# Kernel optimization log

Hardware: AMD Instinct MI355X
Metric: run time of the kernel (lower is better)

Reference implementation:

```python
import jax, jax.numpy as jnp
import numpy as np

D_MODEL = 1024
N_HEADS = 16
HEAD = D_MODEL // N_HEADS
SEQ_THRESH = 64
EPS = 1e-12  # F.normalize eps


def setup_inputs() -> dict:
    key = jax.random.key(0)
    ks = jax.random.split(key, 12)
    B, S = 2, 2048
    scale_init = float(np.log2(SEQ_THRESH ** 2 - SEQ_THRESH))
    return {
        "query": jax.random.normal(ks[0], (B, S, D_MODEL), dtype=jnp.float32),
        "key": jax.random.normal(ks[1], (B, S, D_MODEL), dtype=jnp.float32),
        "value": jax.random.normal(ks[2], (B, S, D_MODEL), dtype=jnp.float32),
        "mask": jax.random.randint(ks[3], (B, S), 0, 2, dtype=jnp.int32),
        "Wq": jax.random.normal(ks[4], (D_MODEL, D_MODEL), dtype=jnp.float32) * (1.0 / np.sqrt(D_MODEL)),
        "bq": jnp.zeros((D_MODEL,), dtype=jnp.float32),
        "Wk": jax.random.normal(ks[5], (D_MODEL, D_MODEL), dtype=jnp.float32) * (1.0 / np.sqrt(D_MODEL)),
        "bk": jnp.zeros((D_MODEL,), dtype=jnp.float32),
        "Wv": jax.random.normal(ks[6], (D_MODEL, D_MODEL), dtype=jnp.float32) * (1.0 / np.sqrt(D_MODEL)),
        "bv": jnp.zeros((D_MODEL,), dtype=jnp.float32),
        "Wo": jax.random.normal(ks[7], (D_MODEL, D_MODEL), dtype=jnp.float32) * (1.0 / np.sqrt(D_MODEL)),
        "bo": jnp.zeros((D_MODEL,), dtype=jnp.float32),
        "scale": jnp.asarray(scale_init, dtype=jnp.float32),
    }


def _split_heads(x):
    B, S, _ = x.shape
    return x.reshape(B, S, N_HEADS, HEAD).transpose(0, 2, 1, 3)  # [B,H,S,hd]


def _center_normalize(x):
    x = x - jnp.mean(x, axis=-1, keepdims=True)
    norm = jnp.linalg.norm(x, axis=-1, keepdims=True)
    return x / jnp.maximum(norm, EPS)


def reference(query, key, value, mask, Wq, bq, Wk, bk, Wv, bv, Wo, bo, scale):
    B, Sq, _ = query.shape
    Q = _split_heads(query @ Wq.T + bq)
    K = _split_heads(key @ Wk.T + bk)
    V = _split_heads(value @ Wv.T + bv)
    Q = _center_normalize(Q)
    K = _center_normalize(K)
    scores = scale * jnp.einsum("bhqd,bhkd->bhqk", Q, K)
    scores = jnp.where(mask[:, None, None, :] == 0, jnp.float32(-1e9), scores)
    attn = jax.nn.softmax(scores, axis=-1)  # [B,H,Sq,Sk]
    ctx = jnp.einsum("bhqk,bhkd->bhqd", attn, V)
    ctx = ctx.transpose(0, 2, 1, 3).reshape(B, Sq, D_MODEL)
    ctx = ctx @ Wo.T + bo
    return (ctx, attn)
```

## Files before the change

kernel.cpp:

```cpp
#include <hip/hip_runtime.h>
#include <math.h>

#define DM   1024
#define NH   16
#define HD   64
#define BATCH 2
#define SEQ  2048
#define MR   (BATCH*SEQ)

typedef __attribute__((ext_vector_type(8))) short bf16x8;
typedef __attribute__((ext_vector_type(4))) float f32x4;

__device__ __forceinline__ unsigned short f2bf(float x) {
    unsigned u = __builtin_bit_cast(unsigned, x);
    u = (u + 0x7FFFu + ((u >> 16) & 1u)) >> 16;
    return (unsigned short)u;
}
__device__ __forceinline__ float bf2f(unsigned short s) {
    unsigned u = ((unsigned)s) << 16;
    return __builtin_bit_cast(float, u);
}

__global__ __launch_bounds__(256) void convert_split(
    const float* __restrict__ src, unsigned short* __restrict__ hi,
    unsigned short* __restrict__ lo, int n4)
{
    int i = blockIdx.x * 256 + threadIdx.x;
    if (i >= n4) return;
    float4 v = ((const float4*)src)[i];
    float f[4] = {v.x, v.y, v.z, v.w};
    unsigned short h[4], l[4];
#pragma unroll
    for (int k = 0; k < 4; ++k) {
        h[k] = f2bf(f[k]);
        l[k] = f2bf(f[k] - bf2f(h[k]));
    }
    ((ushort4*)hi)[i] = make_ushort4(h[0], h[1], h[2], h[3]);
    ((ushort4*)lo)[i] = make_ushort4(l[0], l[1], l[2], l[3]);
}

__global__ __launch_bounds__(256) void convert_single(
    const float* __restrict__ src, unsigned short* __restrict__ dst, int n4)
{
    int i = blockIdx.x * 256 + threadIdx.x;
    if (i >= n4) return;
    float4 v = ((const float4*)src)[i];
    ((ushort4*)dst)[i] = make_ushort4(f2bf(v.x), f2bf(v.y), f2bf(v.z), f2bf(v.w));
}

template<int MODE>
__global__ __launch_bounds__(256) void proj_gemm(
    const unsigned short* __restrict__ Ahi, const unsigned short* __restrict__ Alo,
    const unsigned short* __restrict__ Bhi, const unsigned short* __restrict__ Blo,
    const float* __restrict__ bias,
    void* __restrict__ out0, unsigned short* __restrict__ out1)
{
    __shared__ __align__(16) short As[2][64][40];
    __shared__ __align__(16) short Bs[2][128][40];

    const int tid  = threadIdx.x;
    const int wave = tid >> 6, lane = tid & 63;
    const int quad = lane >> 4, lr = lane & 15;
    const int wy = wave >> 1, wx = wave & 1;
    const int m0 = blockIdx.x * 64, n0 = blockIdx.y * 128;

    f32x4 acc[2][4];
#pragma unroll
    for (int i = 0; i < 2; ++i)
#pragma unroll
        for (int j = 0; j < 4; ++j) acc[i][j] = (f32x4){0.f, 0.f, 0.f, 0.f};

    const int arow = tid >> 2, aseg = (tid & 3) * 8;
    const int brow = tid >> 1, bseg = (tid & 1) * 16;

    for (int k0 = 0; k0 < DM; k0 += 32) {
        __syncthreads();
        {
            const size_t ao = (size_t)(m0 + arow) * DM + k0 + aseg;
            *(uint4*)&As[0][arow][aseg] = *(const uint4*)&Ahi[ao];
            if (MODE == 0)
                *(uint4*)&As[1][arow][aseg] = *(const uint4*)&Alo[ao];
        }
        {
            const size_t bo = (size_t)(n0 + brow) * DM + k0 + bseg;
            *(uint4*)&Bs[0][brow][bseg]     = *(const uint4*)&Bhi[bo];
            *(uint4*)&Bs[0][brow][bseg + 8] = *(const uint4*)&Bhi[bo + 8];
            if (MODE == 0) {
                *(uint4*)&Bs[1][brow][bseg]     = *(const uint4*)&Blo[bo];
                *(uint4*)&Bs[1][brow][bseg + 8] = *(const uint4*)&Blo[bo + 8];
            }
        }
        __syncthreads();
        bf16x8 ah[2], al[2], bh[4], bl[4];
#pragma unroll
        for (int i = 0; i < 2; ++i) {
            ah[i] = *(const bf16x8*)&As[0][wy * 32 + i * 16 + lr][quad * 8];
            if (MODE == 0) al[i] = *(const bf16x8*)&As[1][wy * 32 + i * 16 + lr][quad * 8];
        }
#pragma unroll
        for (int j = 0; j < 4; ++j) {
            bh[j] = *(const bf16x8*)&Bs[0][wx * 64 + j * 16 + lr][quad * 8];
            if (MODE == 0) bl[j] = *(const bf16x8*)&Bs[1][wx * 64 + j * 16 + lr][quad * 8];
        }
#pragma unroll
        for (int i = 0; i < 2; ++i)
#pragma unroll
            for (int j = 0; j < 4; ++j) {
                acc[i][j] = __builtin_amdgcn_mfma_f32_16x16x32_bf16(ah[i], bh[j], acc[i][j], 0, 0, 0);
                if (MODE == 0) {
                    acc[i][j] = __builtin_amdgcn_mfma_f32_16x16x32_bf16(ah[i], bl[j], acc[i][j], 0, 0, 0);
                    acc[i][j] = __builtin_amdgcn_mfma_f32_16x16x32_bf16(al[i], bh[j], acc[i][j], 0, 0, 0);
                }
            }
    }

    float bj[4];
#pragma unroll
    for (int j = 0; j < 4; ++j) bj[j] = bias[n0 + wx * 64 + j * 16 + lr];

    if (MODE == 0) {
        unsigned short* Ohi = (unsigned short*)out0;
#pragma unroll
        for (int i = 0; i < 2; ++i) {
#pragma unroll
            for (int r = 0; r < 4; ++r) {
                float x[4];
#pragma unroll
                for (int j = 0; j < 4; ++j) x[j] = acc[i][j][r] + bj[j];
                float t = x[0] + x[1] + x[2] + x[3];
                t += __shfl_xor(t, 1, 16);
                t += __shfl_xor(t, 2, 16);
                t += __shfl_xor(t, 4, 16);
                t += __shfl_xor(t, 8, 16);
                const float mean = t * (1.0f / 64.0f);
                float ss = 0.f;
#pragma unroll
                for (int j = 0; j < 4; ++j) { x[j] -= mean; ss += x[j] * x[j]; }
                ss += __shfl_xor(ss, 1, 16);
                ss += __shfl_xor(ss, 2, 16);
                ss += __shfl_xor(ss, 4, 16);
                ss += __shfl_xor(ss, 8, 16);
                const float inv = 1.0f / fmaxf(sqrtf(ss), 1e-12f);
                const int row = m0 + wy * 32 + i * 16 + quad * 4 + r;
#pragma unroll
                for (int j = 0; j < 4; ++j) {
                    const float y = x[j] * inv;
                    const unsigned short hh = f2bf(y);
                    const unsigned short ll = f2bf(y - bf2f(hh));
                    const size_t o = (size_t)row * DM + n0 + wx * 64 + j * 16 + lr;
                    Ohi[o]  = hh;
                    out1[o] = ll;
                }
            }
        }
    } else if (MODE == 1) {
        unsigned short* Vg = (unsigned short*)out0;
        const int h = (n0 + wx * 64) >> 6;
#pragma unroll
        for (int i = 0; i < 2; ++i) {
            const int grow = m0 + wy * 32 + i * 16 + quad * 4;
            const int bb = grow >> 11, ss = grow & (SEQ - 1);
#pragma unroll
            for (int j = 0; j < 4; ++j) {
                const int d = j * 16 + lr;
                ushort4 pk;
                pk.x = f2bf(acc[i][j][0] + bj[j]);
                pk.y = f2bf(acc[i][j][1] + bj[j]);
                pk.z = f2bf(acc[i][j][2] + bj[j]);
                pk.w = f2bf(acc[i][j][3] + bj[j]);
                *(ushort4*)&Vg[((size_t)(bb * NH + h) * HD + d) * SEQ + ss] = pk;
            }
        }
    } else {
        float* O = (float*)out0;
#pragma unroll
        for (int i = 0; i < 2; ++i)
#pragma unroll
            for (int j = 0; j < 4; ++j)
#pragma unroll
                for (int r = 0; r < 4; ++r)
                    O[(size_t)(m0 + wy * 32 + i * 16 + quad * 4 + r) * DM +
                      n0 + wx * 64 + j * 16 + lr] = acc[i][j][r] + bj[j];
    }
}

__global__ __launch_bounds__(256) void attn_fused(
    const unsigned short* __restrict__ Qhi, const unsigned short* __restrict__ Qlo,
    const unsigned short* __restrict__ Khi, const unsigned short* __restrict__ Klo,
    const unsigned short* __restrict__ Vg,  const int* __restrict__ mask,
    const float* __restrict__ scale_p,
    float* __restrict__ attn, unsigned short* __restrict__ ctxb)
{
    __shared__ __align__(16) short KHs[64][72];
    __shared__ __align__(16) short KLs[64][72];
    __shared__ __align__(16) short Vs[64][72];
    __shared__ __align__(16) short Ps[64][72];
    __shared__ float mkf[64];

    const int tid = threadIdx.x;
    const int w = tid >> 6, lane = tid & 63;
    const int quad = lane >> 4, lr = lane & 15;

    const int lin = blockIdx.x;
    const int swz = (lin & 7) * 128 + (lin >> 3);
    const int b  = swz >> 9;
    const int h  = (swz >> 5) & 15;
    const int q0 = (swz & 31) * 64;

    const float scl = scale_p[0];
    const float s2 = scl * 1.44269504089f;
    const float c2 = -12.0f * 1.44269504089f;

    const int r0 = tid >> 3,        c0 = (tid & 7) * 8;
    const int r1 = (tid >> 3) + 32, c1 = (tid & 7) * 8;

    {
        const size_t base = ((size_t)(b * SEQ + q0)) * DM + h * HD;
        *(uint4*)&KHs[r0][c0] = *(const uint4*)&Qhi[base + (size_t)r0 * DM + c0];
        *(uint4*)&KHs[r1][c1] = *(const uint4*)&Qhi[base + (size_t)r1 * DM + c1];
        *(uint4*)&KLs[r0][c0] = *(const uint4*)&Qlo[base + (size_t)r0 * DM + c0];
        *(uint4*)&KLs[r1][c1] = *(const uint4*)&Qlo[base + (size_t)r1 * DM + c1];
    }
    __syncthreads();
    bf16x8 qh[2], ql[2];
#pragma unroll
    for (int kc = 0; kc < 2; ++kc) {
        qh[kc] = *(const bf16x8*)&KHs[w * 16 + lr][kc * 32 + quad * 8];
        ql[kc] = *(const bf16x8*)&KLs[w * 16 + lr][kc * 32 + quad * 8];
    }

    float rs[4] = {0.f, 0.f, 0.f, 0.f};

    for (int kt = 0; kt < SEQ / 64; ++kt) {
        const int kk = kt * 64;
        const size_t kb = ((size_t)(b * SEQ + kk)) * DM + h * HD;
        __syncthreads();
        *(uint4*)&KHs[r0][c0] = *(const uint4*)&Khi[kb + (size_t)r0 * DM + c0];
        *(uint4*)&KHs[r1][c1] = *(const uint4*)&Khi[kb + (size_t)r1 * DM + c1];
        *(uint4*)&KLs[r0][c0] = *(const uint4*)&Klo[kb + (size_t)r0 * DM + c0];
        *(uint4*)&KLs[r1][c1] = *(const uint4*)&Klo[kb + (size_t)r1 * DM + c1];
        if (tid < 64) mkf[tid] = mask[b * SEQ + kk + tid] ? c2 : -3.0e38f;
        __syncthreads();
#pragma unroll
        for (int j = 0; j < 4; ++j) {
            bf16x8 bh0 = *(const bf16x8*)&KHs[j * 16 + lr][quad * 8];
            bf16x8 bh1 = *(const bf16x8*)&KHs[j * 16 + lr][32 + quad * 8];
            bf16x8 bl0 = *(const bf16x8*)&KLs[j * 16 + lr][quad * 8];
            bf16x8 bl1 = *(const bf16x8*)&KLs[j * 16 + lr][32 + quad * 8];
            f32x4 sa = (f32x4){0.f, 0.f, 0.f, 0.f};
            sa = __builtin_amdgcn_mfma_f32_16x16x32_bf16(qh[0], bh0, sa, 0, 0, 0);
            sa = __builtin_amdgcn_mfma_f32_16x16x32_bf16(ql[0], bh0, sa, 0, 0, 0);
            sa = __builtin_amdgcn_mfma_f32_16x16x32_bf16(qh[0], bl0, sa, 0, 0, 0);
            sa = __builtin_amdgcn_mfma_f32_16x16x32_bf16(qh[1], bh1, sa, 0, 0, 0);
            sa = __builtin_amdgcn_mfma_f32_16x16x32_bf16(ql[1], bh1, sa, 0, 0, 0);
            sa = __builtin_amdgcn_mfma_f32_16x16x32_bf16(qh[1], bl1, sa, 0, 0, 0);
            const float mo = mkf[j * 16 + lr];
#pragma unroll
            for (int r = 0; r < 4; ++r)
                rs[r] += exp2f(fmaf(sa[r], s2, mo));
        }
    }

    float rinv[4];
#pragma unroll
    for (int r = 0; r < 4; ++r) {
        float t = rs[r];
        t += __shfl_xor(t, 1, 16);
        t += __shfl_xor(t, 2, 16);
        t += __shfl_xor(t, 4, 16);
        t += __shfl_xor(t, 8, 16);
        rinv[r] = 1.0f / fmaxf(t, 1e-30f);
    }

    f32x4 acc_o[4];
#pragma unroll
    for (int dt = 0; dt < 4; ++dt) acc_o[dt] = (f32x4){0.f, 0.f, 0.f, 0.f};

    for (int kt = 0; kt < SEQ / 64; ++kt) {
        const int kk = kt * 64;
        const size_t kb = ((size_t)(b * SEQ + kk)) * DM + h * HD;
        const size_t vb = ((size_t)((b * NH + h) * HD)) * SEQ + kk;
        __syncthreads();
        *(uint4*)&KHs[r0][c0] = *(const uint4*)&Khi[kb + (size_t)r0 * DM + c0];
        *(uint4*)&KHs[r1][c1] = *(const uint4*)&Khi[kb + (size_t)r1 * DM + c1];
        *(uint4*)&KLs[r0][c0] = *(const uint4*)&Klo[kb + (size_t)r0 * DM + c0];
        *(uint4*)&KLs[r1][c1] = *(const uint4*)&Klo[kb + (size_t)r1 * DM + c1];
        *(uint4*)&Vs[r0][c0]  = *(const uint4*)&Vg[vb + (size_t)r0 * SEQ + c0];
        *(uint4*)&Vs[r1][c1]  = *(const uint4*)&Vg[vb + (size_t)r1 * SEQ + c1];
        if (tid < 64) mkf[tid] = mask[b * SEQ + kk + tid] ? c2 : -3.0e38f;
        __syncthreads();
#pragma unroll
        for (int j = 0; j < 4; ++j) {
            bf16x8 bh0 = *(const bf16x8*)&KHs[j * 16 + lr][quad * 8];
            bf16x8 bh1 = *(const bf16x8*)&KHs[j * 16 + lr][32 + quad * 8];
            bf16x8 bl0 = *(const bf16x8*)&KLs[j * 16 + lr][quad * 8];
            bf16x8 bl1 = *(const bf16x8*)&KLs[j * 16 + lr][32 + quad * 8];
            f32x4 sa = (f32x4){0.f, 0.f, 0.f, 0.f};
            sa = __builtin_amdgcn_mfma_f32_16x16x32_bf16(qh[0], bh0, sa, 0, 0, 0);
            sa = __builtin_amdgcn_mfma_f32_16x16x32_bf16(ql[0], bh0, sa, 0, 0, 0);
            sa = __builtin_amdgcn_mfma_f32_16x16x32_bf16(qh[0], bl0, sa, 0, 0, 0);
            sa = __builtin_amdgcn_mfma_f32_16x16x32_bf16(qh[1], bh1, sa, 0, 0, 0);
            sa = __builtin_amdgcn_mfma_f32_16x16x32_bf16(ql[1], bh1, sa, 0, 0, 0);
            sa = __builtin_amdgcn_mfma_f32_16x16x32_bf16(qh[1], bl1, sa, 0, 0, 0);
            const float mo = mkf[j * 16 + lr];
#pragma unroll
            for (int r = 0; r < 4; ++r) {
                const float pn = exp2f(fmaf(sa[r], s2, mo)) * rinv[r];
                const int qrow = q0 + w * 16 + quad * 4 + r;
                attn[((size_t)(b * NH + h) * SEQ + qrow) * SEQ + kk + j * 16 + lr] = pn;
                Ps[w * 16 + quad * 4 + r][j * 16 + lr] = (short)f2bf(pn);
            }
        }
        bf16x8 pa0 = *(const bf16x8*)&Ps[w * 16 + lr][quad * 8];
        bf16x8 pa1 = *(const bf16x8*)&Ps[w * 16 + lr][32 + quad * 8];
#pragma unroll
        for (int dt = 0; dt < 4; ++dt) {
            bf16x8 bv0 = *(const bf16x8*)&Vs[dt * 16 + lr][quad * 8];
            bf16x8 bv1 = *(const bf16x8*)&Vs[dt * 16 + lr][32 + quad * 8];
            acc_o[dt] = __builtin_amdgcn_mfma_f32_16x16x32_bf16(pa0, bv0, acc_o[dt], 0, 0, 0);
            acc_o[dt] = __builtin_amdgcn_mfma_f32_16x16x32_bf16(pa1, bv1, acc_o[dt], 0, 0, 0);
        }
    }

#pragma unroll
    for (int dt = 0; dt < 4; ++dt)
#pragma unroll
        for (int r = 0; r < 4; ++r)
            ctxb[((size_t)(b * SEQ + q0 + w * 16 + quad * 4 + r)) * DM +
                 h * HD + dt * 16 + lr] = (unsigned short)f2bf(acc_o[dt][r]);
}

extern "C" void kernel_launch(void* const* d_in, const int* in_sizes, int n_in,
                              void* d_out, int out_size, void* d_ws, size_t ws_size,
                              hipStream_t stream)
{
    const float* query = (const float*)d_in[0];
    const float* key   = (const float*)d_in[1];
    const float* value = (const float*)d_in[2];
    const int*   mask  = (const int*)d_in[3];
    const float* Wq = (const float*)d_in[4];
    const float* bq = (const float*)d_in[5];
    const float* Wk = (const float*)d_in[6];
    const float* bk = (const float*)d_in[7];
    const float* Wv = (const float*)d_in[8];
    const float* bv = (const float*)d_in[9];
    const float* Wo = (const float*)d_in[10];
    const float* bo = (const float*)d_in[11];
    const float* scale = (const float*)d_in[12];

    float* out_ctx  = (float*)d_out;
    float* out_attn = out_ctx + (size_t)MR * DM;

    const size_t WSZ = (size_t)DM * DM;
    const size_t TSZ = (size_t)MR * DM;
    unsigned short* p = (unsigned short*)d_ws;
    unsigned short* Wq_hi = p; p += WSZ;
    unsigned short* Wq_lo = p; p += WSZ;
    unsigned short* Wk_hi = p; p += WSZ;
    unsigned short* Wk_lo = p; p += WSZ;
    unsigned short* Wv_b  = p; p += WSZ;
    unsigned short* Wo_b  = p; p += WSZ;
    unsigned short* Qn_hi = p; p += TSZ;
    unsigned short* Qn_lo = p; p += TSZ;
    unsigned short* Kn_hi = p; p += TSZ;
    unsigned short* Kn_lo = p; p += TSZ;
    unsigned short* Vg    = p; p += TSZ;
    unsigned short* ctxb  = Wq_hi;
    unsigned short* Ahi = (unsigned short*)out_attn;
    unsigned short* Alo = Ahi + TSZ;

    convert_split <<<1024, 256, 0, stream>>>(Wq, Wq_hi, Wq_lo, 262144);
    convert_split <<<1024, 256, 0, stream>>>(Wk, Wk_hi, Wk_lo, 262144);
    convert_single<<<1024, 256, 0, stream>>>(Wv, Wv_b, 262144);
    convert_single<<<1024, 256, 0, stream>>>(Wo, Wo_b, 262144);

    dim3 gg(MR / 64, DM / 128);

    convert_split <<<4096, 256, 0, stream>>>(query, Ahi, Alo, (int)(TSZ / 4));
    proj_gemm<0><<<gg, 256, 0, stream>>>(Ahi, Alo, Wq_hi, Wq_lo, bq, Qn_hi, Qn_lo);
    convert_split <<<4096, 256, 0, stream>>>(key, Ahi, Alo, (int)(TSZ / 4));
    proj_gemm<0><<<gg, 256, 0, stream>>>(Ahi, Alo, Wk_hi, Wk_lo, bk, Kn_hi, Kn_lo);
    convert_single<<<4096, 256, 0, stream>>>(value, Ahi, (int)(TSZ / 4));
    proj_gemm<1><<<gg, 256, 0, stream>>>(Ahi, nullptr, Wv_b, nullptr, bv, Vg, nullptr);

    attn_fused<<<dim3(SEQ / 64 * NH * BATCH), 256, 0, stream>>>(
        Qn_hi, Qn_lo, Kn_hi, Kn_lo, Vg, mask, scale, out_attn, ctxb);

    proj_gemm<2><<<gg, 256, 0, stream>>>(ctxb, nullptr, Wo_b, nullptr, bo, out_ctx, nullptr);
}
```

Measured before the change: 920.2 us.

## Fuse two-pass attention into one pass with deferred normalization and register prefetch

```diff
diff --git a/kernel.cpp b/kernel.cpp
--- a/kernel.cpp
+++ b/kernel.cpp
@@ -189,12 +189,13 @@
     const unsigned short* __restrict__ Khi, const unsigned short* __restrict__ Klo,
     const unsigned short* __restrict__ Vg,  const int* __restrict__ mask,
     const float* __restrict__ scale_p,
-    float* __restrict__ attn, unsigned short* __restrict__ ctxb)
+    float* __restrict__ attn, unsigned short* __restrict__ ctxb,
+    float* __restrict__ rowinv_g)
 {
     __shared__ __align__(16) short KHs[64][72];
     __shared__ __align__(16) short KLs[64][72];
     __shared__ __align__(16) short Vs[64][72];
-    __shared__ __align__(16) short Ps[64][72];
+    __shared__ __align__(16) short Ps[64][68];
     __shared__ float mkf[64];
 
     const int tid = threadIdx.x;
@@ -230,17 +231,48 @@
     }
 
     float rs[4] = {0.f, 0.f, 0.f, 0.f};
-
-    for (int kt = 0; kt < SEQ / 64; ++kt) {
+    f32x4 acc_o[4];
+#pragma unroll
+    for (int dt = 0; dt < 4; ++dt) acc_o[dt] = (f32x4){0.f, 0.f, 0.f, 0.f};
+
+    uint4 pKH0, pKH1, pKL0, pKL1, pV0, pV1;
+    int pmk = 0;
+
+    auto load_tile = [&](int kt) {
         const int kk = kt * 64;
         const size_t kb = ((size_t)(b * SEQ + kk)) * DM + h * HD;
-        __syncthreads();
-        *(uint4*)&KHs[r0][c0] = *(const uint4*)&Khi[kb + (size_t)r0 * DM + c0];
-        *(uint4*)&KHs[r1][c1] = *(const uint4*)&Khi[kb + (size_t)r1 * DM + c1];
-        *(uint4*)&KLs[r0][c0] = *(const uint4*)&Klo[kb + (size_t)r0 * DM + c0];
-        *(uint4*)&KLs[r1][c1] = *(const uint4*)&Klo[kb + (size_t)r1 * DM + c1];
-        if (tid < 64) mkf[tid] = mask[b * SEQ + kk + tid] ? c2 : -3.0e38f;
-        __syncthreads();
+        const size_t vb = ((size_t)((b * NH + h) * HD)) * SEQ + kk;
+        pKH0 = *(const uint4*)&Khi[kb + (size_t)r0 * DM + c0];
+        pKH1 = *(const uint4*)&Khi[kb + (size_t)r1 * DM + c1];
+        pKL0 = *(const uint4*)&Klo[kb + (size_t)r0 * DM + c0];
+        pKL1 = *(const uint4*)&Klo[kb + (size_t)r1 * DM + c1];
+        pV0  = *(const uint4*)&Vg[vb + (size_t)r0 * SEQ + c0];
+        pV1  = *(const uint4*)&Vg[vb + (size_t)r1 * SEQ + c1];
+        if (tid < 64) pmk = mask[b * SEQ + kk + tid];
+    };
+
+    load_tile(0);
+
+    for (int kt = 0; kt < SEQ / 64; ++kt) {
+        asm volatile("s_waitcnt lgkmcnt(0)" ::: "memory");
+        __builtin_amdgcn_s_barrier();
+        __builtin_amdgcn_sched_barrier(0);
+
+        *(uint4*)&KHs[r0][c0] = pKH0;
+        *(uint4*)&KHs[r1][c1] = pKH1;
+        *(uint4*)&KLs[r0][c0] = pKL0;
+        *(uint4*)&KLs[r1][c1] = pKL1;
+        *(uint4*)&Vs[r0][c0]  = pV0;
+        *(uint4*)&Vs[r1][c1]  = pV1;
+        if (tid < 64) mkf[tid] = pmk ? c2 : -3.0e38f;
+
+        if (kt + 1 < SEQ / 64) load_tile(kt + 1);
+
+        asm volatile("s_waitcnt lgkmcnt(0)" ::: "memory");
+        __builtin_amdgcn_s_barrier();
+        __builtin_amdgcn_sched_barrier(0);
+
+        const int kk = kt * 64;
 #pragma unroll
         for (int j = 0; j < 4; ++j) {
             bf16x8 bh0 = *(const bf16x8*)&KHs[j * 16 + lr][quad * 8];
@@ -248,17 +280,35 @@
             bf16x8 bl0 = *(const bf16x8*)&KLs[j * 16 + lr][quad * 8];
             bf16x8 bl1 = *(const bf16x8*)&KLs[j * 16 + lr][32 + quad * 8];
             f32x4 sa = (f32x4){0.f, 0.f, 0.f, 0.f};
+            __builtin_amdgcn_s_setprio(1);
             sa = __builtin_amdgcn_mfma_f32_16x16x32_bf16(qh[0], bh0, sa, 0, 0, 0);
             sa = __builtin_amdgcn_mfma_f32_16x16x32_bf16(ql[0], bh0, sa, 0, 0, 0);
             sa = __builtin_amdgcn_mfma_f32_16x16x32_bf16(qh[0], bl0, sa, 0, 0, 0);
             sa = __builtin_amdgcn_mfma_f32_16x16x32_bf16(qh[1], bh1, sa, 0, 0, 0);
             sa = __builtin_amdgcn_mfma_f32_16x16x32_bf16(ql[1], bh1, sa, 0, 0, 0);
             sa = __builtin_amdgcn_mfma_f32_16x16x32_bf16(qh[1], bl1, sa, 0, 0, 0);
+            __builtin_amdgcn_s_setprio(0);
             const float mo = mkf[j * 16 + lr];
 #pragma unroll
-            for (int r = 0; r < 4; ++r)
-                rs[r] += exp2f(fmaf(sa[r], s2, mo));
-        }
+            for (int r = 0; r < 4; ++r) {
+                const float e = exp2f(fmaf(sa[r], s2, mo));
+                rs[r] += e;
+                const int qrow = q0 + w * 16 + quad * 4 + r;
+                attn[((size_t)(b * NH + h) * SEQ + qrow) * SEQ + kk + j * 16 + lr] = e;
+                Ps[w * 16 + quad * 4 + r][j * 16 + lr] = (short)f2bf(e);
+            }
+        }
+        bf16x8 pa0 = *(const bf16x8*)&Ps[w * 16 + lr][quad * 8];
+        bf16x8 pa1 = *(const bf16x8*)&Ps[w * 16 + lr][32 + quad * 8];
+        __builtin_amdgcn_s_setprio(1);
+#pragma unroll
+        for (int dt = 0; dt < 4; ++dt) {
+            bf16x8 bv0 = *(const bf16x8*)&Vs[dt * 16 + lr][quad * 8];
+            bf16x8 bv1 = *(const bf16x8*)&Vs[dt * 16 + lr][32 + quad * 8];
+            acc_o[dt] = __builtin_amdgcn_mfma_f32_16x16x32_bf16(pa0, bv0, acc_o[dt], 0, 0, 0);
+            acc_o[dt] = __builtin_amdgcn_mfma_f32_16x16x32_bf16(pa1, bv1, acc_o[dt], 0, 0, 0);
+        }
+        __builtin_amdgcn_s_setprio(0);
     }
 
     float rinv[4];
@@ -271,56 +321,15 @@
         t += __shfl_xor(t, 8, 16);
         rinv[r] = 1.0f / fmaxf(t, 1e-30f);
     }
-
-    f32x4 acc_o[4];
-#pragma unroll
-    for (int dt = 0; dt < 4; ++dt) acc_o[dt] = (f32x4){0.f, 0.f, 0.f, 0.f};
-
-    for (int kt = 0; kt < SEQ / 64; ++kt) {
-        const int kk = kt * 64;
-        const size_t kb = ((size_t)(b * SEQ + kk)) * DM + h * HD;
-        const size_t vb = ((size_t)((b * NH + h) * HD)) * SEQ + kk;
-        __syncthreads();
-        *(uint4*)&KHs[r0][c0] = *(const uint4*)&Khi[kb + (size_t)r0 * DM + c0];
-        *(uint4*)&KHs[r1][c1] = *(const uint4*)&Khi[kb + (size_t)r1 * DM + c1];
-        *(uint4*)&KLs[r0][c0] = *(const uint4*)&Klo[kb + (size_t)r0 * DM + c0];
-        *(uint4*)&KLs[r1][c1] = *(const uint4*)&Klo[kb + (size_t)r1 * DM + c1];
-        *(uint4*)&Vs[r0][c0]  = *(const uint4*)&Vg[vb + (size_t)r0 * SEQ + c0];
-        *(uint4*)&Vs[r1][c1]  = *(const uint4*)&Vg[vb + (size_t)r1 * SEQ + c1];
-        if (tid < 64) mkf[tid] = mask[b * SEQ + kk + tid] ? c2 : -3.0e38f;
-        __syncthreads();
-#pragma unroll
-        for (int j = 0; j < 4; ++j) {
-            bf16x8 bh0 = *(const bf16x8*)&KHs[j * 16 + lr][quad * 8];
-            bf16x8 bh1 = *(const bf16x8*)&KHs[j * 16 + lr][32 + quad * 8];
-            bf16x8 bl0 = *(const bf16x8*)&KLs[j * 16 + lr][quad * 8];
-            bf16x8 bl1 = *(const bf16x8*)&KLs[j * 16 + lr][32 + quad * 8];
-            f32x4 sa = (f32x4){0.f, 0.f, 0.f, 0.f};
-            sa = __builtin_amdgcn_mfma_f32_16x16x32_bf16(qh[0], bh0, sa, 0, 0, 0);
-            sa = __builtin_amdgcn_mfma_f32_16x16x32_bf16(ql[0], bh0, sa, 0, 0, 0);
-            sa = __builtin_amdgcn_mfma_f32_16x16x32_bf16(qh[0], bl0, sa, 0, 0, 0);
-            sa = __builtin_amdgcn_mfma_f32_16x16x32_bf16(qh[1], bh1, sa, 0, 0, 0);
-            sa = __builtin_amdgcn_mfma_f32_16x16x32_bf16(ql[1], bh1, sa, 0, 0, 0);
-            sa = __builtin_amdgcn_mfma_f32_16x16x32_bf16(qh[1], bl1, sa, 0, 0, 0);
-            const float mo = mkf[j * 16 + lr];
-#pragma unroll
-            for (int r = 0; r < 4; ++r) {
-                const float pn = exp2f(fmaf(sa[r], s2, mo)) * rinv[r];
-                const int qrow = q0 + w * 16 + quad * 4 + r;
-                attn[((size_t)(b * NH + h) * SEQ + qrow) * SEQ + kk + j * 16 + lr] = pn;
-                Ps[w * 16 + quad * 4 + r][j * 16 + lr] = (short)f2bf(pn);
-            }
-        }
-        bf16x8 pa0 = *(const bf16x8*)&Ps[w * 16 + lr][quad * 8];
-        bf16x8 pa1 = *(const bf16x8*)&Ps[w * 16 + lr][32 + quad * 8];
-#pragma unroll
-        for (int dt = 0; dt < 4; ++dt) {
-            bf16x8 bv0 = *(const bf16x8*)&Vs[dt * 16 + lr][quad * 8];
-            bf16x8 bv1 = *(const bf16x8*)&Vs[dt * 16 + lr][32 + quad * 8];
-            acc_o[dt] = __builtin_amdgcn_mfma_f32_16x16x32_bf16(pa0, bv0, acc_o[dt], 0, 0, 0);
-            acc_o[dt] = __builtin_amdgcn_mfma_f32_16x16x32_bf16(pa1, bv1, acc_o[dt], 0, 0, 0);
-        }
-    }
+    if (lr == 0) {
+        const size_t base = (size_t)(b * NH + h) * SEQ + q0 + w * 16 + quad * 4;
+#pragma unroll
+        for (int r = 0; r < 4; ++r) rowinv_g[base + r] = rinv[r];
+    }
+#pragma unroll
+    for (int dt = 0; dt < 4; ++dt)
+#pragma unroll
+        for (int r = 0; r < 4; ++r) acc_o[dt][r] *= rinv[r];
 
 #pragma unroll
     for (int dt = 0; dt < 4; ++dt)
@@ -328,6 +337,20 @@
         for (int r = 0; r < 4; ++r)
             ctxb[((size_t)(b * SEQ + q0 + w * 16 + quad * 4 + r)) * DM +
                  h * HD + dt * 16 + lr] = (unsigned short)f2bf(acc_o[dt][r]);
+}
+
+__global__ __launch_bounds__(256) void rescale_attn(
+    float* __restrict__ attn, const float* __restrict__ rowinv)
+{
+    const size_t N4 = (size_t)BATCH * NH * SEQ * (SEQ / 4);
+    size_t i = (size_t)blockIdx.x * 256 + threadIdx.x;
+    const size_t stride = (size_t)gridDim.x * 256;
+    for (; i < N4; i += stride) {
+        float4 v = ((float4*)attn)[i];
+        const float s = rowinv[i >> 9];
+        v.x *= s; v.y *= s; v.z *= s; v.w *= s;
+        ((float4*)attn)[i] = v;
+    }
 }
 
 extern "C" void kernel_launch(void* const* d_in, const int* in_sizes, int n_in,
@@ -368,6 +391,7 @@
     unsigned short* ctxb  = Wq_hi;
     unsigned short* Ahi = (unsigned short*)out_attn;
     unsigned short* Alo = Ahi + TSZ;
+    float* rowinv = out_ctx;
 
     convert_split <<<1024, 256, 0, stream>>>(Wq, Wq_hi, Wq_lo, 262144);
     convert_split <<<1024, 256, 0, stream>>>(Wk, Wk_hi, Wk_lo, 262144);
@@ -384,7 +408,9 @@
     proj_gemm<1><<<gg, 256, 0, stream>>>(Ahi, nullptr, Wv_b, nullptr, bv, Vg, nullptr);
 
     attn_fused<<<dim3(SEQ / 64 * NH * BATCH), 256, 0, stream>>>(
-        Qn_hi, Qn_lo, Kn_hi, Kn_lo, Vg, mask, scale, out_attn, ctxb);
+        Qn_hi, Qn_lo, Kn_hi, Kn_lo, Vg, mask, scale, out_attn, ctxb, rowinv);
+
+    rescale_attn<<<4096, 256, 0, stream>>>(out_attn, rowinv);
 
     proj_gemm<2><<<gg, 256, 0, stream>>>(ctxb, nullptr, Wo_b, nullptr, bo, out_ctx, nullptr);
 }
```

New measurement: 1.061 ms. 15.3% more time.
